# Performance work log

Hardware: AMD Instinct MI355X
Metric: run time of the kernel (lower is better)

## Reference

```python
import jax, jax.numpy as jnp
import numpy as np

N = 50000; E = 800000; G = 256; F = 34; D = 128; H = 4; C = 32; L = 4
EPS = 1e-5

def _bn(x, g, b):
    # BatchNorm1d with batch statistics (train-mode math), eval dropout (identity)
    m = jnp.mean(x, 0); v = jnp.var(x, 0)
    return g * (x - m) * jax.lax.rsqrt(v + EPS) + b

def _seg_softmax(s, seg, n):
    # numerically-stable softmax over edges grouped by destination node
    m = jax.ops.segment_max(s, seg, num_segments=n)
    m = jnp.where(jnp.isfinite(m), m, 0.0)
    e = jnp.exp(s - m[seg])
    d = jax.ops.segment_sum(e, seg, num_segments=n)
    return e / (d[seg] + 1e-16)

def setup_inputs():
    key = jax.random.key(0)
    ks = iter(jax.random.split(key, 64))
    def rn(shape, s=0.05):
        return jax.random.normal(next(ks), shape, dtype=jnp.float32) * s
    inp = {}
    inp['x'] = jax.random.normal(next(ks), (N, F), dtype=jnp.float32)
    inp['edge_index'] = jax.random.randint(next(ks), (2, E), 0, N, dtype=jnp.int32)
    inp['batch'] = jnp.sort(jax.random.randint(next(ks), (N,), 0, G, dtype=jnp.int32))
    inp['emb_W'] = rn((F, D)); inp['emb_b'] = rn((D,))
    inp['emb_g'] = jnp.ones((D,)); inp['emb_be'] = jnp.zeros((D,))
    inp['gWl'] = rn((L, D, D)); inp['gWr'] = rn((L, D, D))
    inp['gbl'] = rn((L, D)); inp['gbr'] = rn((L, D))
    inp['gatt'] = rn((L, H, C)); inp['gbias'] = rn((L, D))
    inp['gg'] = jnp.ones((L, D)); inp['gbe'] = jnp.zeros((L, D))
    inp['tWq'] = rn((D, D)); inp['tWk'] = rn((D, D)); inp['tWv'] = rn((D, D)); inp['tWs'] = rn((D, D))
    inp['tbq'] = rn((D,)); inp['tbk'] = rn((D,)); inp['tbv'] = rn((D,)); inp['tbs'] = rn((D,))
    inp['tg'] = jnp.ones((D,)); inp['tbe'] = jnp.zeros((D,))
    inp['oW1'] = rn((2 * D, D)); inp['ob1'] = rn((D,))
    inp['og'] = jnp.ones((D,)); inp['obe'] = jnp.zeros((D,))
    inp['oW2'] = rn((D, D // 2)); inp['ob2'] = rn((D // 2,))
    inp['oW3'] = rn((D // 2, 1)); inp['ob3'] = rn((1,))
    return inp

def reference(x, edge_index, batch, emb_W, emb_b, emb_g, emb_be, gWl, gWr, gbl, gbr, gatt, gbias, gg, gbe, tWq, tWk, tWv, tWs, tbq, tbk, tbv, tbs, tg, tbe, oW1, ob1, og, obe, oW2, ob2, oW3, ob3):
    x = jax.nn.relu(_bn(x @ emb_W + emb_b, emb_g, emb_be))
    sl = jnp.arange(N, dtype=edge_index.dtype)
    ei = jnp.concatenate([edge_index, jnp.stack([sl, sl])], axis=1)  # GATv2 default add_self_loops=True
    src, dst = ei[0], ei[1]
    for l in range(L):  # 4 structurally identical GATv2 layers
        xl = (x @ gWl[l] + gbl[l]).reshape(N, H, C)
        xr = (x @ gWr[l] + gbr[l]).reshape(N, H, C)
        e = jax.nn.leaky_relu(xl[src] + xr[dst], 0.2)  # [E+N, H, C]
        sc = jnp.einsum('ehc,hc->eh', e, gatt[l])
        a = _seg_softmax(sc, dst, N)
        out = jax.ops.segment_sum(xl[src] * a[..., None], dst, num_segments=N).reshape(N, D) + gbias[l]
        x = x + jax.nn.relu(_bn(out, gg[l], gbe[l]))
    # TransformerConv: no self-loops by default, dot-product attention + root skip
    s2, d2 = edge_index[0], edge_index[1]
    q = (x @ tWq + tbq).reshape(N, H, C)
    k = (x @ tWk + tbk).reshape(N, H, C)
    v = (x @ tWv + tbv).reshape(N, H, C)
    sc = jnp.einsum('ehc,ehc->eh', q[d2], k[s2]) / np.float32(np.sqrt(C))
    a = _seg_softmax(sc, d2, N)
    agg = jax.ops.segment_sum(v[s2] * a[..., None], d2, num_segments=N).reshape(N, D)
    x = x + _bn(agg + x @ tWs + tbs, tg, tbe)
    # global mean + max pooling over graphs
    cnt = jax.ops.segment_sum(jnp.ones((N,), x.dtype), batch, num_segments=G)
    xm = jax.ops.segment_sum(x, batch, num_segments=G) / jnp.maximum(cnt, 1.0)[:, None]
    xx = jax.ops.segment_max(x, batch, num_segments=G)
    xx = jnp.where(jnp.isfinite(xx), xx, 0.0)  # guard empty segments
    h = jnp.concatenate([xm, xx], axis=1)
    h = jax.nn.relu(_bn(h @ oW1 + ob1, og, obe))
    h = jax.nn.relu(h @ oW2 + ob2)
    return h @ oW3 + ob3
```

## Files before the change

### kernel.cpp

```cpp
#include <hip/hip_runtime.h>
#include <hip/hip_fp16.h>

namespace {
constexpr int NN = 50000;
constexpr int NE = 800000;
constexpr int NG = 256;
constexpr int NF = 34;
constexpr int NL = 4;
constexpr int NB = (NN + 255) / 256;
constexpr int STS = 32;
}
#define EPSB 1e-5f
#define LSLOPE 0.2f
#define INV_SQRT_C 0.17677669529663687f

typedef short bf16x8 __attribute__((ext_vector_type(8)));
typedef float f32x4 __attribute__((ext_vector_type(4)));
typedef _Float16 hv2 __attribute__((ext_vector_type(2)));

static __device__ __forceinline__ short f2bf(float f) {
    unsigned int u = __float_as_uint(f);
    u = (u + 0x7fff + ((u >> 16) & 1)) >> 16;
    return (short)u;
}
static __device__ __forceinline__ unsigned fenc(float x) {
    unsigned u = __float_as_uint(x);
    return (u & 0x80000000u) ? ~u : (u | 0x80000000u);
}
static __device__ __forceinline__ float fdec(unsigned u) {
    return __uint_as_float((u & 0x80000000u) ? (u ^ 0x80000000u) : ~u);
}
static __device__ __forceinline__ float fdot2(hv2 a, hv2 b, float c) {
    return __builtin_amdgcn_fdot2(a, b, c, false);
}

__global__ __launch_bounds__(256) void k_deg(const int* __restrict__ ei,
                                             int* __restrict__ deg,
                                             int* __restrict__ rank) {
    int tid = blockIdx.x * 256 + threadIdx.x;
    const int S = (NE + 3) / 4;
    if (tid >= S) return;
#pragma unroll
    for (int k = 0; k < 4; ++k) {
        int e = tid + k * S;
        if (e < NE) rank[e] = atomicAdd(&deg[ei[NE + e]], 1);
    }
}

__global__ __launch_bounds__(256) void k_scan1(const int* __restrict__ deg, int* __restrict__ bsum) {
    __shared__ int sm[256];
    int i = blockIdx.x * 256 + threadIdx.x;
    sm[threadIdx.x] = (i < NN) ? deg[i] : 0;
    __syncthreads();
    for (int off = 128; off > 0; off >>= 1) {
        if (threadIdx.x < off) sm[threadIdx.x] += sm[threadIdx.x + off];
        __syncthreads();
    }
    if (threadIdx.x == 0) bsum[blockIdx.x] = sm[0];
}

__global__ __launch_bounds__(256) void k_scan2(const int* __restrict__ bsum,
// ... 38 lines not shown
    int tid = blockIdx.x * 256 + threadIdx.x;
    const int S = (NE + 3) / 4;
    if (tid >= S) return;
#pragma unroll
    for (int k = 0; k < 4; ++k) {
        int e = tid + k * S;
        if (e < NE) {
            int s = ei[e];
            int d = ei[NE + e];
            int p = rp[d] + rank[e];
            esrc[p] = s;
        }
    }
}

__global__ __launch_bounds__(256) void k_prep(const float* __restrict__ gWl,
                                              const float* __restrict__ gWr,
                                              const float* __restrict__ tWq,
                                              const float* __restrict__ tWk,
                                              const float* __restrict__ tWv,
                                              const float* __restrict__ tWs,
                                              short* __restrict__ dst) {
    int m = blockIdx.x;
    const float* src;
    if (m < 4) src = gWl + m * 16384;
    else if (m < 8) src = gWr + (m - 4) * 16384;
    else if (m == 8) src = tWq;
    else if (m == 9) src = tWk;
    else if (m == 10) src = tWv;
    else src = tWs;
    short* d = dst + m * 16384;
    for (int i = threadIdx.x; i < 16384; i += 256) {
        int n = i >> 7, k = i & 127;
        d[i] = f2bf(src[k * 128 + n]);
    }
}

__global__ __launch_bounds__(256) void k_stats(const float* __restrict__ src, int nRows,
                                               float* __restrict__ st) {
    int c = threadIdx.x & 127;
    int sub = threadIdx.x >> 7;
    int r0 = blockIdx.x * 128;
    int rend = r0 + 128; if (rend > nRows) rend = nRows;
    float s = 0.f, ss = 0.f;
    for (int r = r0 + sub; r < rend; r += 2) {
        float v = src[(size_t)r * 128 + c];
        s += v; ss += v * v;
    }
    float* dst = st + (blockIdx.x & (STS - 1)) * 256;
    atomicAdd(&dst[c], s);
    atomicAdd(&dst[128 + c], ss);
}

template <int OUTH0, int OUTH1, int RES, int XOUT>
__global__ __launch_bounds__(256) void k_gemm2bn(const float* __restrict__ src,
                                                 const float* __restrict__ res,
                                                 float* __restrict__ xout,
                                                 const float* __restrict__ st,
                                                 const float* __restrict__ g,
                                                 const float* __restrict__ b,
                                                 const short* __restrict__ Wt0,
                                                 const short* __restrict__ Wt1,
                                                 const float* __restrict__ bias0,
                                                 const float* __restrict__ bias1,
                                                 void* __restrict__ out0,
                                                 void* __restrict__ out1, int nRows) {
    __shared__ short As[128 * 136];
    __shared__ short Bs[128 * 136];
    __shared__ float scsh[256];
    const float invn = 1.f / NN;
    if (threadIdx.x < 128) {
        int c = threadIdx.x;
        float s0v = 0.f, s1v = 0.f;
#pragma unroll 8
        for (int k2 = 0; k2 < STS; ++k2) {
            s0v += st[k2 * 256 + c];
            s1v += st[k2 * 256 + 128 + c];
        }
        float mean = s0v * invn;
        float var = fmaxf(s1v * invn - mean * mean, 0.f);
        float s = g[c] * rsqrtf(var + EPSB);
        scsh[c] = s;
        scsh[128 + c] = b[c] - mean * s;
    }
    {
        const int4* Wt4 = (const int4*)Wt0;
        for (int idx = threadIdx.x; idx < 2048; idx += 256) {
            int row = idx >> 4, c8 = idx & 15;
            *(int4*)&Bs[row * 136 + c8 * 8] = Wt4[idx];
        }
    }
    __syncthreads();
    int r0 = blockIdx.x * 128;
    int rows = nRows - r0; if (rows > 128) rows = 128;
    for (int idx = threadIdx.x; idx < 2048; idx += 256) {
        int r = idx >> 4, c8 = idx & 15;
        short4 sa = {0, 0, 0, 0}, sb = {0, 0, 0, 0};
        if (r < rows) {
            size_t base = (size_t)(r0 + r) * 128 + c8 * 8;
            float4 v0 = *(const float4*)&src[base];
            float4 v1 = *(const float4*)&src[base + 4];
            int c = c8 * 8;
            v0.x = fmaxf(v0.x * scsh[c + 0] + scsh[128 + c + 0], 0.f);
            v0.y = fmaxf(v0.y * scsh[c + 1] + scsh[128 + c + 1], 0.f);
            v0.z = fmaxf(v0.z * scsh[c + 2] + scsh[128 + c + 2], 0.f);
            v0.w = fmaxf(v0.w * scsh[c + 3] + scsh[128 + c + 3], 0.f);
            v1.x = fmaxf(v1.x * scsh[c + 4] + scsh[128 + c + 4], 0.f);
            v1.y = fmaxf(v1.y * scsh[c + 5] + scsh[128 + c + 5], 0.f);
            v1.z = fmaxf(v1.z * scsh[c + 6] + scsh[128 + c + 6], 0.f);
            v1.w = fmaxf(v1.w * scsh[c + 7] + scsh[128 + c + 7], 0.f);
            if (RES) {
                float4 rr0 = *(const float4*)&res[base];
                float4 rr1 = *(const float4*)&res[base + 4];
                v0.x += rr0.x; v0.y += rr0.y; v0.z += rr0.z; v0.w += rr0.w;
                v1.x += rr1.x; v1.y += rr1.y; v1.z += rr1.z; v1.w += rr1.w;
            }
            if (XOUT) {
                *(float4*)&xout[base] = v0;
                *(float4*)&xout[base + 4] = v1;
            }
            sa.x = f2bf(v0.x); sa.y = f2bf(v0.y); sa.z = f2bf(v0.z); sa.w = f2bf(v0.w);
            sb.x = f2bf(v1.x); sb.y = f2bf(v1.y); sb.z = f2bf(v1.z); sb.w = f2bf(v1.w);
        }
        *(short4*)&As[r * 136 + c8 * 8] = sa;
        *(short4*)&As[r * 136 + c8 * 8 + 4] = sb;
    }
    __syncthreads();
    int lane = threadIdx.x & 63, wave = threadIdx.x >> 6;
    int n16 = lane & 15, quad = lane >> 4;
    bf16x8 af[2][4];
#pragma unroll
    for (int rt = 0; rt < 2; ++rt)
#pragma unroll
        for (int kc = 0; kc < 4; ++kc)
            af[rt][kc] = *(const bf16x8*)&As[(wave * 32 + rt * 16 + n16) * 136 + kc * 32 + quad * 8];

    f32x4 acc[2][8];
#pragma unroll
    for (int rt = 0; rt < 2; ++rt)
#pragma unroll
        for (int ct = 0; ct < 8; ++ct) acc[rt][ct] = (f32x4){0.f, 0.f, 0.f, 0.f};
#pragma unroll
    for (int ct = 0; ct < 8; ++ct)
#pragma unroll
        for (int kc = 0; kc < 4; ++kc) {
            bf16x8 bf = *(const bf16x8*)&Bs[(ct * 16 + n16) * 136 + kc * 32 + quad * 8];
            acc[0][ct] = __builtin_amdgcn_mfma_f32_16x16x32_bf16(af[0][kc], bf, acc[0][ct], 0, 0, 0);
            acc[1][ct] = __builtin_amdgcn_mfma_f32_16x16x32_bf16(af[1][kc], bf, acc[1][ct], 0, 0, 0);
        }
#pragma unroll
    for (int ct = 0; ct < 8; ++ct) {
        int colI = ct * 16 + n16;
        float bv = bias0[colI];
#pragma unroll
        for (int rt = 0; rt < 2; ++rt)
#pragma unroll
            for (int reg = 0; reg < 4; ++reg) {
                int r = wave * 32 + rt * 16 + quad * 4 + reg;
                if (r < rows) {
                    float v = acc[rt][ct][reg] + bv;
                    if (OUTH0) ((__half*)out0)[(size_t)(r0 + r) * 128 + colI] = __float2half(v);
                    else       ((float*)out0)[(size_t)(r0 + r) * 128 + colI] = v;
                }
            }
    }
    __syncthreads();
    {
        const int4* Wt4 = (const int4*)Wt1;
        for (int idx = threadIdx.x; idx < 2048; idx += 256) {
            int row = idx >> 4, c8 = idx & 15;
            *(int4*)&Bs[row * 136 + c8 * 8] = Wt4[idx];
        }
    }
    __syncthreads();
#pragma unroll
    for (int rt = 0; rt < 2; ++rt)
#pragma unroll
        for (int ct = 0; ct < 8; ++ct) acc[rt][ct] = (f32x4){0.f, 0.f, 0.f, 0.f};
#pragma unroll
    for (int ct = 0; ct < 8; ++ct)
#pragma unroll
        for (int kc = 0; kc < 4; ++kc) {
            bf16x8 bf = *(const bf16x8*)&Bs[(ct * 16 + n16) * 136 + kc * 32 + quad * 8];
            acc[0][ct] = __builtin_amdgcn_mfma_f32_16x16x32_bf16(af[0][kc], bf, acc[0][ct], 0, 0, 0);
            acc[1][ct] = __builtin_amdgcn_mfma_f32_16x16x32_bf16(af[1][kc], bf, acc[1][ct], 0, 0, 0);
        }
#pragma unroll
    for (int ct = 0; ct < 8; ++ct) {
        int colI = ct * 16 + n16;
        float bv = bias1[colI];
#pragma unroll
        for (int rt = 0; rt < 2; ++rt)
#pragma unroll
            for (int reg = 0; reg < 4; ++reg) {
                int r = wave * 32 + rt * 16 + quad * 4 + reg;
                if (r < rows) {
                    float v = acc[rt][ct][reg] + bv;
                    if (OUTH1) ((__half*)out1)[(size_t)(r0 + r) * 128 + colI] = __float2half(v);
                    else       ((float*)out1)[(size_t)(r0 + r) * 128 + colI] = v;
                }
            }
    }
}

__global__ __launch_bounds__(256) void k_gemm4bn(const float* __restrict__ src,
                                                 const float* __restrict__ res,
                                                 float* __restrict__ xout,
                                                 const float* __restrict__ st,
                                                 const float* __restrict__ g,
                                                 const float* __restrict__ b,
                                                 const short* __restrict__ Wt,
                                                 const float* __restrict__ bq,
                                                 const float* __restrict__ bk,
                                                 const float* __restrict__ bv,
                                                 const float* __restrict__ bs,
                                                 __half* __restrict__ oq,
                                                 __half* __restrict__ ok,
                                                 __half* __restrict__ ov,
                                                 __half* __restrict__ os, int nRows) {
    __shared__ short As[128 * 136];
    __shared__ short Bs[128 * 136];
    __shared__ float scsh[256];
    const float invn = 1.f / NN;
    if (threadIdx.x < 128) {
        int c = threadIdx.x;
        float s0v = 0.f, s1v = 0.f;
#pragma unroll 8
        for (int k2 = 0; k2 < STS; ++k2) {
            s0v += st[k2 * 256 + c];
            s1v += st[k2 * 256 + 128 + c];
        }
        float mean = s0v * invn;
        float var = fmaxf(s1v * invn - mean * mean, 0.f);
        float s = g[c] * rsqrtf(var + EPSB);
        scsh[c] = s;
        scsh[128 + c] = b[c] - mean * s;
    }
    __syncthreads();
    int r0 = blockIdx.x * 128;
    int rows = nRows - r0; if (rows > 128) rows = 128;
    for (int idx = threadIdx.x; idx < 2048; idx += 256) {
        int r = idx >> 4, c8 = idx & 15;
        short4 sa = {0, 0, 0, 0}, sb = {0, 0, 0, 0};
        if (r < rows) {
            size_t base = (size_t)(r0 + r) * 128 + c8 * 8;
            float4 v0 = *(const float4*)&src[base];
            float4 v1 = *(const float4*)&src[base + 4];
            int c = c8 * 8;
            v0.x = fmaxf(v0.x * scsh[c + 0] + scsh[128 + c + 0], 0.f);
            v0.y = fmaxf(v0.y * scsh[c + 1] + scsh[128 + c + 1], 0.f);
            v0.z = fmaxf(v0.z * scsh[c + 2] + scsh[128 + c + 2], 0.f);
            v0.w = fmaxf(v0.w * scsh[c + 3] + scsh[128 + c + 3], 0.f);
            v1.x = fmaxf(v1.x * scsh[c + 4] + scsh[128 + c + 4], 0.f);
            v1.y = fmaxf(v1.y * scsh[c + 5] + scsh[128 + c + 5], 0.f);
            v1.z = fmaxf(v1.z * scsh[c + 6] + scsh[128 + c + 6], 0.f);
            v1.w = fmaxf(v1.w * scsh[c + 7] + scsh[128 + c + 7], 0.f);
            float4 rr0 = *(const float4*)&res[base];
            float4 rr1 = *(const float4*)&res[base + 4];
            v0.x += rr0.x; v0.y += rr0.y; v0.z += rr0.z; v0.w += rr0.w;
            v1.x += rr1.x; v1.y += rr1.y; v1.z += rr1.z; v1.w += rr1.w;
            *(float4*)&xout[base] = v0;
            *(float4*)&xout[base + 4] = v1;
            sa.x = f2bf(v0.x); sa.y = f2bf(v0.y); sa.z = f2bf(v0.z); sa.w = f2bf(v0.w);
            sb.x = f2bf(v1.x); sb.y = f2bf(v1.y); sb.z = f2bf(v1.z); sb.w = f2bf(v1.w);
        }
        *(short4*)&As[r * 136 + c8 * 8] = sa;
        *(short4*)&As[r * 136 + c8 * 8 + 4] = sb;
    }
    int lane = threadIdx.x & 63, wave = threadIdx.x >> 6;
    int n16 = lane & 15, quad = lane >> 4;
    __half* outs[4] = {oq, ok, ov, os};
    const float* biases[4] = {bq, bk, bv, bs};
    bf16x8 af[2][4];
    bool afLoaded = false;
    for (int m = 0; m < 4; ++m) {
        {
            const int4* Wt4 = (const int4*)(Wt + (size_t)m * 16384);
            for (int idx = threadIdx.x; idx < 2048; idx += 256) {
                int row = idx >> 4, c8 = idx & 15;
                *(int4*)&Bs[row * 136 + c8 * 8] = Wt4[idx];
            }
        }
        __syncthreads();
        if (!afLoaded) {
            afLoaded = true;
#pragma unroll
            for (int rt = 0; rt < 2; ++rt)
#pragma unroll
                for (int kc = 0; kc < 4; ++kc)
                    af[rt][kc] = *(const bf16x8*)&As[(wave * 32 + rt * 16 + n16) * 136 + kc * 32 + quad * 8];
        }
        f32x4 acc[2][8];
#pragma unroll
        for (int rt = 0; rt < 2; ++rt)
#pragma unroll
            for (int ct = 0; ct < 8; ++ct) acc[rt][ct] = (f32x4){0.f, 0.f, 0.f, 0.f};
#pragma unroll
        for (int ct = 0; ct < 8; ++ct)
#pragma unroll
            for (int kc = 0; kc < 4; ++kc) {
                bf16x8 bf = *(const bf16x8*)&Bs[(ct * 16 + n16) * 136 + kc * 32 + quad * 8];
                acc[0][ct] = __builtin_amdgcn_mfma_f32_16x16x32_bf16(af[0][kc], bf, acc[0][ct], 0, 0, 0);
                acc[1][ct] = __builtin_amdgcn_mfma_f32_16x16x32_bf16(af[1][kc], bf, acc[1][ct], 0, 0, 0);
            }
        __half* om = outs[m];
        const float* bm = biases[m];
#pragma unroll
        for (int ct = 0; ct < 8; ++ct) {
            int colI = ct * 16 + n16;
            float bv2 = bm[colI];
#pragma unroll
            for (int rt = 0; rt < 2; ++rt)
#pragma unroll
                for (int reg = 0; reg < 4; ++reg) {
                    int r = wave * 32 + rt * 16 + quad * 4 + reg;
                    if (r < rows)
                        om[(size_t)(r0 + r) * 128 + colI] = __float2half(acc[rt][ct][reg] + bv2);
                }
        }
        if (m < 3) __syncthreads();
    }
}

__global__ __launch_bounds__(256) void k_gemm_emb(const float* __restrict__ A,
                                                  const float* __restrict__ W,
                                                  const float* __restrict__ bias,
                                                  float* __restrict__ out, int nRows,
                                                  float* __restrict__ stms) {
    __shared__ float As[64 * NF];
    __shared__ float sred[256];
    int r0 = blockIdx.x * 64;
    int rows = nRows - r0; if (rows > 64) rows = 64;
    int total = rows * NF;
    for (int idx = threadIdx.x; idx < 64 * NF; idx += 256)
        As[idx] = (idx < total) ? A[(size_t)r0 * NF + idx] : 0.f;
    sred[threadIdx.x] = 0.f;
    __syncthreads();
    int tx = threadIdx.x & 31, ty = threadIdx.x >> 5;
    const float4* W4 = (const float4*)W;
    float acc[8][4];
#pragma unroll
    for (int j = 0; j < 8; ++j)
#pragma unroll
        for (int i = 0; i < 4; ++i) acc[j][i] = 0.f;
#pragma unroll 2
    for (int k = 0; k < NF; ++k) {
        float4 w = W4[k * 32 + tx];
#pragma unroll
        for (int j = 0; j < 8; ++j) {
            float a = As[(ty * 8 + j) * NF + k];
            acc[j][0] += a * w.x; acc[j][1] += a * w.y;
            acc[j][2] += a * w.z; acc[j][3] += a * w.w;
        }
    }
    float4 b = ((const float4*)bias)[tx];
    float s[4] = {0.f, 0.f, 0.f, 0.f}, ss[4] = {0.f, 0.f, 0.f, 0.f};
#pragma unroll
    for (int j = 0; j < 8; ++j) {
        int r = ty * 8 + j;
        if (r < rows) {
            float4 o = make_float4(acc[j][0] + b.x, acc[j][1] + b.y,
                                   acc[j][2] + b.z, acc[j][3] + b.w);
            ((float4*)out)[(size_t)(r0 + r) * 32 + tx] = o;
            s[0] += o.x; ss[0] += o.x * o.x;
            s[1] += o.y; ss[1] += o.y * o.y;
            s[2] += o.z; ss[2] += o.z * o.z;
            s[3] += o.w; ss[3] += o.w * o.w;
        }
    }
#pragma unroll
    for (int i = 0; i < 4; ++i) {
        atomicAdd(&sred[tx * 4 + i], s[i]);
        atomicAdd(&sred[128 + tx * 4 + i], ss[i]);
    }
    __syncthreads();
    atomicAdd(&stms[(blockIdx.x & (STS - 1)) * 256 + threadIdx.x], sred[threadIdx.x]);
}

__global__ __launch_bounds__(256) void k_gat_aggr(const __half* __restrict__ xl,
                                                  const __half* __restrict__ xr,
                                                  const float* __restrict__ att,
                                                  const float* __restrict__ gbias_l,
                                                  const int* __restrict__ rp,
                                                  const int* __restrict__ esrc,
                                                  float* __restrict__ out) {
    int lane = threadIdx.x & 63;
    int node = blockIdx.x * 4 + (threadIdx.x >> 6);
    if (node >= NN) return;
    int q = lane >> 4;
    int l16 = lane & 15;
    int c8 = l16 * 8;
    float4 xrr = *(const float4*)&xr[(unsigned)node * 128u + c8];
    hv2 xrh[4] = {*(hv2*)&xrr.x, *(hv2*)&xrr.y, *(hv2*)&xrr.z, *(hv2*)&xrr.w};
    float4 atA = *(const float4*)&att[c8];
    float4 atB = *(const float4*)&att[c8 + 4];
    hv2 ath[4] = {{(_Float16)atA.x, (_Float16)atA.y}, {(_Float16)atA.z, (_Float16)atA.w},
                  {(_Float16)atB.x, (_Float16)atB.y}, {(_Float16)atB.z, (_Float16)atB.w}};
    const hv2 hz = {(_Float16)0.f, (_Float16)0.f};
    const hv2 hs = {(_Float16)LSLOPE, (_Float16)LSLOPE};
    int s0 = rp[node];
// ... 20 lines not shown
            a[2 * k + 1] += w * (float)f[k].y;
        }
        l += w;
    };
    int j = q;
    for (; j + 12 < T; j += 16) { body(j); body(j + 4); body(j + 8); body(j + 12); }
    for (; j + 4 < T; j += 8) { body(j); body(j + 4); }
    for (; j < T; j += 4) body(j);
#pragma unroll
    for (int k = 0; k < 8; ++k) { a[k] += __shfl_xor(a[k], 16); a[k] += __shfl_xor(a[k], 32); }
    l += __shfl_xor(l, 16); l += __shfl_xor(l, 32);
    if (q == 0) {
        float inv = 1.f / (l + 1e-16f);
        float4 gb0 = *(const float4*)&gbias_l[c8];
        float4 gb1 = *(const float4*)&gbias_l[c8 + 4];
        float4 o0 = make_float4(a[0] * inv + gb0.x, a[1] * inv + gb0.y,
                                a[2] * inv + gb0.z, a[3] * inv + gb0.w);
        float4 o1 = make_float4(a[4] * inv + gb1.x, a[5] * inv + gb1.y,
                                a[6] * inv + gb1.z, a[7] * inv + gb1.w);
        *(float4*)&out[(unsigned)node * 128u + c8] = o0;
        *(float4*)&out[(unsigned)node * 128u + c8 + 4] = o1;
    }
}

__global__ __launch_bounds__(256) void k_trans_aggr(const __half* __restrict__ qh,
                                                    const __half* __restrict__ kh,
                                                    const __half* __restrict__ vv,
                                                    const __half* __restrict__ sT,
                                                    const int* __restrict__ rp,
                                                    const int* __restrict__ esrc,
                                                    float* __restrict__ out) {
    int lane = threadIdx.x & 63;
    int node = blockIdx.x * 4 + (threadIdx.x >> 6);
    if (node >= NN) return;
    int q = lane >> 4;
    int l16 = lane & 15;
    int c8 = l16 * 8;
    float4 qr = *(const float4*)&qh[(unsigned)node * 128u + c8];
    const hv2 hinv = {(_Float16)INV_SQRT_C, (_Float16)INV_SQRT_C};
    hv2 qv[4] = {(*(hv2*)&qr.x) * hinv, (*(hv2*)&qr.y) * hinv,
                 (*(hv2*)&qr.z) * hinv, (*(hv2*)&qr.w) * hinv};
    int s0 = rp[node];
    int T = rp[node + 1] - s0;
    float a[8] = {0.f, 0.f, 0.f, 0.f, 0.f, 0.f, 0.f, 0.f};
    float l = 0.f;
    auto body = [&](int j) {
// ... 13 lines not shown
            a[2 * k + 1] += w * (float)vvv[k].y;
        }
        l += w;
    };
    int j = q;
    for (; j + 12 < T; j += 16) { body(j); body(j + 4); body(j + 8); body(j + 12); }
    for (; j + 4 < T; j += 8) { body(j); body(j + 4); }
    for (; j < T; j += 4) body(j);
#pragma unroll
    for (int k = 0; k < 8; ++k) { a[k] += __shfl_xor(a[k], 16); a[k] += __shfl_xor(a[k], 32); }
    l += __shfl_xor(l, 16); l += __shfl_xor(l, 32);
    if (q == 0) {
        float inv = 1.f / (l + 1e-16f);
        float4 straw = *(const float4*)&sT[(unsigned)node * 128u + c8];
        hv2 st[4] = {*(hv2*)&straw.x, *(hv2*)&straw.y, *(hv2*)&straw.z, *(hv2*)&straw.w};
        float4 o0 = make_float4(a[0] * inv + (float)st[0].x, a[1] * inv + (float)st[0].y,
                                a[2] * inv + (float)st[1].x, a[3] * inv + (float)st[1].y);
        float4 o1 = make_float4(a[4] * inv + (float)st[2].x, a[5] * inv + (float)st[2].y,
                                a[6] * inv + (float)st[3].x, a[7] * inv + (float)st[3].y);
        *(float4*)&out[(unsigned)node * 128u + c8] = o0;
        *(float4*)&out[(unsigned)node * 128u + c8 + 4] = o1;
    }
}

__global__ __launch_bounds__(256) void k_pool_part(const float* __restrict__ src,
                                                   const float* __restrict__ res,
                                                   const float* __restrict__ st,
                                                   const float* __restrict__ g,
                                                   const float* __restrict__ b,
                                                   const int* __restrict__ batch,
                                                   float* __restrict__ psum,
                                                   unsigned* __restrict__ pmax) {
    __shared__ int bs[64];
    __shared__ float sc_sh[128], sh_sh[128];
    int r0 = blockIdx.x * 64;
    if (threadIdx.x < 64) {
        int r = r0 + threadIdx.x;
        bs[threadIdx.x] = (r < NN) ? batch[r] : -1;
    }
    const float invn = 1.f / NN;
// ... 17 lines not shown
    float scv = sc_sh[c];
    float shv = sh_sh[c];
    int curg = -1;
    float s = 0.f, fmx = -INFINITY;
    for (int i = sub; i < 64; i += 2) {
        int r = r0 + i;
        if (r >= NN) break;
        int gr = bs[i];
        if (gr != curg) {
            if (curg >= 0) {
                atomicAdd(&psum[curg * 128 + c], s);
                atomicMax(&pmax[curg * 128 + c], fenc(fmx));
            }
            curg = gr; s = 0.f; fmx = -INFINITY;
        }
        float v = src[(size_t)r * 128 + c] * scv + shv + res[(size_t)r * 128 + c];
        s += v; fmx = fmaxf(fmx, v);
    }
    if (curg >= 0) {
        atomicAdd(&psum[curg * 128 + c], s);
        atomicMax(&pmax[curg * 128 + c], fenc(fmx));
    }
}

__global__ __launch_bounds__(128) void k_pool_head1(const float* __restrict__ psum,
                                                    const unsigned* __restrict__ pmax,
                                                    const int* __restrict__ batch,
                                                    const float* __restrict__ W,
                                                    const float* __restrict__ b,
                                                    float* __restrict__ t1,
                                                    float* __restrict__ st6) {
// ... 106 lines not shown
    __half* xrh  = xlh + NDsz;
    __half* vh   = xrh + NDsz;
    __half* sh   = vh + NDsz;
    short* Wt    = (short*)(sh + NDsz);
    int* deg     = (int*)(Wt + 12 * 16384);
    int* rp      = deg + NN;
    int* cursor  = rp + NN + 1;
    int2* edg    = (int2*)(cursor + NN);
    int* bsum    = (int*)(edg + NE + 64);
    int* boff    = bsum + 256;
    float* psum  = (float*)(boff + 256);
    unsigned* pmax = (unsigned*)(psum + NG * 128);
    int* rank    = (int*)scb;
    int* esrc    = (int*)edg;
    float* stms  = scb + NE;

    hipMemsetAsync(deg, 0, NN * sizeof(int), stream);
    hipMemsetAsync(stats + 6 * 256, 0, 256 * sizeof(float), stream);
    hipMemsetAsync(stms, 0, 6 * STS * 256 * sizeof(float), stream);
    hipMemsetAsync(psum, 0, NG * 128 * 2 * sizeof(float), stream);

    k_prep<<<12, 256, 0, stream>>>(gWl, gWr, tWq, tWk, tWv, tWs, Wt);

    const int S4 = (NE + 3) / 4;
    const int gQuarter = (S4 + 255) / 256;
    k_deg<<<gQuarter, 256, 0, stream>>>(ei, deg, rank);
    k_scan1<<<NB, 256, 0, stream>>>(deg, bsum);
    k_scan2<<<1, 256, 0, stream>>>(bsum, boff, rp);
    k_scan3<<<NB, 256, 0, stream>>>(deg, boff, rp);
    k_fill<<<gQuarter, 256, 0, stream>>>(ei, rp, rank, esrc);

    const int gEmb  = (NN + 63) / 64;
    const int gGemm = (NN + 127) / 128;
    const int gStat = (NN + 127) / 128;
    const int gNode = (NN + 3) / 4;
    const int gPool = (NN + 63) / 64;
    const int REG = STS * 256;

    k_gemm_emb<<<gEmb, 256, 0, stream>>>(x_in, emb_W, emb_b, bA, NN, stms + 0 * REG);

    k_gemm2bn<1, 1, 0, 1><<<gGemm, 256, 0, stream>>>(bA, nullptr, x, stms + 0 * REG, emb_g, emb_be,
                                                     Wt + (size_t)0 * 16384, Wt + (size_t)4 * 16384,
                                                     gbl + 0 * 128, gbr + 0 * 128, xlh, xrh, NN);
    k_gat_aggr<<<gNode, 256, 0, stream>>>(xlh, xrh, gatt + 0 * 128, gbias + 0 * 128, rp, esrc, bC);
    k_stats<<<gStat, 256, 0, stream>>>(bC, NN, stms + 1 * REG);
    k_gemm2bn<1, 1, 1, 1><<<gGemm, 256, 0, stream>>>(bC, x, bA, stms + 1 * REG, gg + 0 * 128, gbe + 0 * 128,
                                                     Wt + (size_t)1 * 16384, Wt + (size_t)5 * 16384,
                                                     gbl + 1 * 128, gbr + 1 * 128, xlh, xrh, NN);
    k_gat_aggr<<<gNode, 256, 0, stream>>>(xlh, xrh, gatt + 1 * 128, gbias + 1 * 128, rp, esrc, bC);
    k_stats<<<gStat, 256, 0, stream>>>(bC, NN, stms + 2 * REG);
    k_gemm2bn<1, 1, 1, 1><<<gGemm, 256, 0, stream>>>(bC, bA, x, stms + 2 * REG, gg + 1 * 128, gbe + 1 * 128,
                                                     Wt + (size_t)2 * 16384, Wt + (size_t)6 * 16384,
                                                     gbl + 2 * 128, gbr + 2 * 128, xlh, xrh, NN);
    k_gat_aggr<<<gNode, 256, 0, stream>>>(xlh, xrh, gatt + 2 * 128, gbias + 2 * 128, rp, esrc, bC);
    k_stats<<<gStat, 256, 0, stream>>>(bC, NN, stms + 3 * REG);
    k_gemm2bn<1, 1, 1, 1><<<gGemm, 256, 0, stream>>>(bC, x, bA, stms + 3 * REG, gg + 2 * 128, gbe + 2 * 128,
                                                     Wt + (size_t)3 * 16384, Wt + (size_t)7 * 16384,
                                                     gbl + 3 * 128, gbr + 3 * 128, xlh, xrh, NN);
    k_gat_aggr<<<gNode, 256, 0, stream>>>(xlh, xrh, gatt + 3 * 128, gbias + 3 * 128, rp, esrc, bC);
    k_stats<<<gStat, 256, 0, stream>>>(bC, NN, stms + 4 * REG);

    k_gemm4bn<<<gGemm, 256, 0, stream>>>(bC, bA, x, stms + 4 * REG, gg + 3 * 128, gbe + 3 * 128,
                                         Wt + (size_t)8 * 16384, tbq, tbk, tbv, tbs,
                                         xrh, xlh, vh, sh, NN);
    k_trans_aggr<<<gNode, 256, 0, stream>>>(xrh, xlh, vh, sh, rp, esrc, bC);
    k_stats<<<gStat, 256, 0, stream>>>(bC, NN, stms + 5 * REG);

    k_pool_part<<<gPool, 256, 0, stream>>>(bC, x, stms + 5 * REG, tg, tbe, batch, psum, pmax);
    k_pool_head1<<<NG, 128, 0, stream>>>(psum, pmax, batch, oW1, ob1, t1, stats + 6 * 256);
    k_head2<<<NG, 64, 0, stream>>>(t1, stats + 6 * 256, og, obe, oW2, ob2, oW3, ob3, out);
}
```

Measured before the change: 821.8 us.

## Store aggregation outputs in fp16, halve GEMM row tiles, merge init kernels

```diff
diff --git a/kernel.cpp b/kernel.cpp
--- a/kernel.cpp
+++ b/kernel.cpp
@@ -9,6 +9,8 @@
 constexpr int NL = 4;
 constexpr int NB = (NN + 255) / 256;
 constexpr int STS = 32;
+constexpr int GQ = ((NE + 3) / 4 + 255) / 256;
+constexpr int GE = (NN + 63) / 64;
 }
 #define EPSB 1e-5f
 #define LSLOPE 0.2f
@@ -34,17 +36,98 @@
     return __builtin_amdgcn_fdot2(a, b, c, false);
 }
 
-__global__ __launch_bounds__(256) void k_deg(const int* __restrict__ ei,
-                                             int* __restrict__ deg,
-                                             int* __restrict__ rank) {
-    int tid = blockIdx.x * 256 + threadIdx.x;
-    const int S = (NE + 3) / 4;
-    if (tid >= S) return;
-#pragma unroll
-    for (int k = 0; k < 4; ++k) {
-        int e = tid + k * S;
-        if (e < NE) rank[e] = atomicAdd(&deg[ei[NE + e]], 1);
-    }
+__global__ __launch_bounds__(256) void k_init(const int* __restrict__ ei,
+                                              int* __restrict__ deg,
+                                              int* __restrict__ rank,
+                                              const float* __restrict__ gWl,
+                                              const float* __restrict__ gWr,
+                                              const float* __restrict__ tWq,
+                                              const float* __restrict__ tWk,
+                                              const float* __restrict__ tWv,
+                                              const float* __restrict__ tWs,
+                                              short* __restrict__ Wt,
+                                              const float* __restrict__ A,
+                                              const float* __restrict__ W,
+                                              const float* __restrict__ bias,
+                                              float* __restrict__ outEmb,
+                                              float* __restrict__ stms) {
+    __shared__ float As[64 * NF];
+    __shared__ float sred[256];
+    int blk = blockIdx.x;
+    if (blk < GQ) {
+        int tid = blk * 256 + threadIdx.x;
+        const int S = (NE + 3) / 4;
+        if (tid >= S) return;
+#pragma unroll
+        for (int k = 0; k < 4; ++k) {
+            int e = tid + k * S;
+            if (e < NE) rank[e] = atomicAdd(&deg[ei[NE + e]], 1);
+        }
+        return;
+    }
+    blk -= GQ;
+    if (blk < 12) {
+        const float* src;
+        if (blk < 4) src = gWl + blk * 16384;
+        else if (blk < 8) src = gWr + (blk - 4) * 16384;
+        else if (blk == 8) src = tWq;
+        else if (blk == 9) src = tWk;
+        else if (blk == 10) src = tWv;
+        else src = tWs;
+        short* d = Wt + blk * 16384;
+        for (int i = threadIdx.x; i < 16384; i += 256) {
+            int n = i >> 7, k = i & 127;
+            d[i] = f2bf(src[k * 128 + n]);
+        }
+        return;
+    }
+    blk -= 12;
+    int r0 = blk * 64;
+    int rows = NN - r0; if (rows > 64) rows = 64;
+    int total = rows * NF;
+    for (int idx = threadIdx.x; idx < 64 * NF; idx += 256)
+        As[idx] = (idx < total) ? A[(size_t)r0 * NF + idx] : 0.f;
+    sred[threadIdx.x] = 0.f;
+    __syncthreads();
+    int tx = threadIdx.x & 31, ty = threadIdx.x >> 5;
+    const float4* W4 = (const float4*)W;
+    float acc[8][4];
+#pragma unroll
+    for (int j = 0; j < 8; ++j)
+#pragma unroll
+        for (int i = 0; i < 4; ++i) acc[j][i] = 0.f;
+#pragma unroll 2
+    for (int k = 0; k < NF; ++k) {
+        float4 w = W4[k * 32 + tx];
+#pragma unroll
+        for (int j = 0; j < 8; ++j) {
+            float a = As[(ty * 8 + j) * NF + k];
+            acc[j][0] += a * w.x; acc[j][1] += a * w.y;
+            acc[j][2] += a * w.z; acc[j][3] += a * w.w;
+        }
+    }
+    float4 b = ((const float4*)bias)[tx];
+    float s[4] = {0.f, 0.f, 0.f, 0.f}, ss[4] = {0.f, 0.f, 0.f, 0.f};
+#pragma unroll
+    for (int j = 0; j < 8; ++j) {
+        int r = ty * 8 + j;
+        if (r < rows) {
+            float4 o = make_float4(acc[j][0] + b.x, acc[j][1] + b.y,
+                                   acc[j][2] + b.z, acc[j][3] + b.w);
+            ((float4*)outEmb)[(size_t)(r0 + r) * 32 + tx] = o;
+            s[0] += o.x; ss[0] += o.x * o.x;
+            s[1] += o.y; ss[1] += o.y * o.y;
+            s[2] += o.z; ss[2] += o.z * o.z;
+            s[3] += o.w; ss[3] += o.w * o.w;
+        }
+    }
+#pragma unroll
+    for (int i = 0; i < 4; ++i) {
+        atomicAdd(&sred[tx * 4 + i], s[i]);
+        atomicAdd(&sred[128 + tx * 4 + i], ss[i]);
+    }
+    __syncthreads();
+    atomicAdd(&stms[(blk & (STS - 1)) * 256 + threadIdx.x], sred[threadIdx.x]);
 }
 
 __global__ __launch_bounds__(256) void k_scan1(const int* __restrict__ deg, int* __restrict__ bsum) {
@@ -113,29 +196,7 @@
     }
 }
 
-__global__ __launch_bounds__(256) void k_prep(const float* __restrict__ gWl,
-                                              const float* __restrict__ gWr,
-                                              const float* __restrict__ tWq,
-                                              const float* __restrict__ tWk,
-                                              const float* __restrict__ tWv,
-                                              const float* __restrict__ tWs,
-                                              short* __restrict__ dst) {
-    int m = blockIdx.x;
-    const float* src;
-    if (m < 4) src = gWl + m * 16384;
-    else if (m < 8) src = gWr + (m - 4) * 16384;
-    else if (m == 8) src = tWq;
-    else if (m == 9) src = tWk;
-    else if (m == 10) src = tWv;
-    else src = tWs;
-    short* d = dst + m * 16384;
-    for (int i = threadIdx.x; i < 16384; i += 256) {
-        int n = i >> 7, k = i & 127;
-        d[i] = f2bf(src[k * 128 + n]);
-    }
-}
-
-__global__ __launch_bounds__(256) void k_stats(const float* __restrict__ src, int nRows,
+__global__ __launch_bounds__(256) void k_stats(const __half* __restrict__ src, int nRows,
                                                float* __restrict__ st) {
     int c = threadIdx.x & 127;
     int sub = threadIdx.x >> 7;
@@ -143,7 +204,7 @@
     int rend = r0 + 128; if (rend > nRows) rend = nRows;
     float s = 0.f, ss = 0.f;
     for (int r = r0 + sub; r < rend; r += 2) {
-        float v = src[(size_t)r * 128 + c];
+        float v = __half2float(src[(size_t)r * 128 + c]);
         s += v; ss += v * v;
     }
     float* dst = st + (blockIdx.x & (STS - 1)) * 256;
@@ -151,7 +212,7 @@
     atomicAdd(&dst[128 + c], ss);
 }
 
-template <int OUTH0, int OUTH1, int RES, int XOUT>
+template <int SRC16, int OUTH0, int OUTH1, int RES, int XOUT>
 __global__ __launch_bounds__(256) void k_gemm2bn(const float* __restrict__ src,
                                                  const float* __restrict__ res,
                                                  float* __restrict__ xout,
@@ -164,7 +225,7 @@
                                                  const float* __restrict__ bias1,
                                                  void* __restrict__ out0,
                                                  void* __restrict__ out1, int nRows) {
-    __shared__ short As[128 * 136];
+    __shared__ short As[64 * 136];
     __shared__ short Bs[128 * 136];
     __shared__ float scsh[256];
     const float invn = 1.f / NN;
@@ -190,15 +251,25 @@
         }
     }
     __syncthreads();
-    int r0 = blockIdx.x * 128;
-    int rows = nRows - r0; if (rows > 128) rows = 128;
-    for (int idx = threadIdx.x; idx < 2048; idx += 256) {
+    int r0 = blockIdx.x * 64;
+    int rows = nRows - r0; if (rows > 64) rows = 64;
+    for (int idx = threadIdx.x; idx < 1024; idx += 256) {
         int r = idx >> 4, c8 = idx & 15;
         short4 sa = {0, 0, 0, 0}, sb = {0, 0, 0, 0};
         if (r < rows) {
             size_t base = (size_t)(r0 + r) * 128 + c8 * 8;
-            float4 v0 = *(const float4*)&src[base];
-            float4 v1 = *(const float4*)&src[base + 4];
+            float4 v0, v1;
+            if (SRC16) {
+                union { float4 f4; __half h[8]; } u;
+                u.f4 = *(const float4*)&((const __half*)src)[base];
+                v0 = make_float4(__half2float(u.h[0]), __half2float(u.h[1]),
+                                 __half2float(u.h[2]), __half2float(u.h[3]));
+                v1 = make_float4(__half2float(u.h[4]), __half2float(u.h[5]),
+                                 __half2float(u.h[6]), __half2float(u.h[7]));
+            } else {
+                v0 = *(const float4*)&src[base];
+                v1 = *(const float4*)&src[base + 4];
+            }
             int c = c8 * 8;
             v0.x = fmaxf(v0.x * scsh[c + 0] + scsh[128 + c + 0], 0.f);
             v0.y = fmaxf(v0.y * scsh[c + 1] + scsh[128 + c + 1], 0.f);
@@ -227,41 +298,34 @@
     __syncthreads();
     int lane = threadIdx.x & 63, wave = threadIdx.x >> 6;
     int n16 = lane & 15, quad = lane >> 4;
-    bf16x8 af[2][4];
-#pragma unroll
-    for (int rt = 0; rt < 2; ++rt)
-#pragma unroll
-        for (int kc = 0; kc < 4; ++kc)
-            af[rt][kc] = *(const bf16x8*)&As[(wave * 32 + rt * 16 + n16) * 136 + kc * 32 + quad * 8];
-
-    f32x4 acc[2][8];
-#pragma unroll
-    for (int rt = 0; rt < 2; ++rt)
-#pragma unroll
-        for (int ct = 0; ct < 8; ++ct) acc[rt][ct] = (f32x4){0.f, 0.f, 0.f, 0.f};
+    bf16x8 af[4];
+#pragma unroll
+    for (int kc = 0; kc < 4; ++kc)
+        af[kc] = *(const bf16x8*)&As[(wave * 16 + n16) * 136 + kc * 32 + quad * 8];
+
+    f32x4 acc[8];
+#pragma unroll
+    for (int ct = 0; ct < 8; ++ct) acc[ct] = (f32x4){0.f, 0.f, 0.f, 0.f};
 #pragma unroll
     for (int ct = 0; ct < 8; ++ct)
 #pragma unroll
         for (int kc = 0; kc < 4; ++kc) {
             bf16x8 bf = *(const bf16x8*)&Bs[(ct * 16 + n16) * 136 + kc * 32 + quad * 8];
-            acc[0][ct] = __builtin_amdgcn_mfma_f32_16x16x32_bf16(af[0][kc], bf, acc[0][ct], 0, 0, 0);
-            acc[1][ct] = __builtin_amdgcn_mfma_f32_16x16x32_bf16(af[1][kc], bf, acc[1][ct], 0, 0, 0);
+            acc[ct] = __builtin_amdgcn_mfma_f32_16x16x32_bf16(af[kc], bf, acc[ct], 0, 0, 0);
         }
 #pragma unroll
     for (int ct = 0; ct < 8; ++ct) {
         int colI = ct * 16 + n16;
         float bv = bias0[colI];
 #pragma unroll
-        for (int rt = 0; rt < 2; ++rt)
-#pragma unroll
-            for (int reg = 0; reg < 4; ++reg) {
-                int r = wave * 32 + rt * 16 + quad * 4 + reg;
-                if (r < rows) {
-                    float v = acc[rt][ct][reg] + bv;
-                    if (OUTH0) ((__half*)out0)[(size_t)(r0 + r) * 128 + colI] = __float2half(v);
-                    else       ((float*)out0)[(size_t)(r0 + r) * 128 + colI] = v;
-                }
+        for (int reg = 0; reg < 4; ++reg) {
+            int r = wave * 16 + quad * 4 + reg;
+            if (r < rows) {
+                float v = acc[ct][reg] + bv;
+                if (OUTH0) ((__half*)out0)[(size_t)(r0 + r) * 128 + colI] = __float2half(v);
+                else       ((float*)out0)[(size_t)(r0 + r) * 128 + colI] = v;
             }
+        }
     }
     __syncthreads();
     {
@@ -273,36 +337,31 @@
     }
     __syncthreads();
 #pragma unroll
-    for (int rt = 0; rt < 2; ++rt)
-#pragma unroll
-        for (int ct = 0; ct < 8; ++ct) acc[rt][ct] = (f32x4){0.f, 0.f, 0.f, 0.f};
+    for (int ct = 0; ct < 8; ++ct) acc[ct] = (f32x4){0.f, 0.f, 0.f, 0.f};
 #pragma unroll
     for (int ct = 0; ct < 8; ++ct)
 #pragma unroll
         for (int kc = 0; kc < 4; ++kc) {
             bf16x8 bf = *(const bf16x8*)&Bs[(ct * 16 + n16) * 136 + kc * 32 + quad * 8];
-            acc[0][ct] = __builtin_amdgcn_mfma_f32_16x16x32_bf16(af[0][kc], bf, acc[0][ct], 0, 0, 0);
-            acc[1][ct] = __builtin_amdgcn_mfma_f32_16x16x32_bf16(af[1][kc], bf, acc[1][ct], 0, 0, 0);
+            acc[ct] = __builtin_amdgcn_mfma_f32_16x16x32_bf16(af[kc], bf, acc[ct], 0, 0, 0);
         }
 #pragma unroll
     for (int ct = 0; ct < 8; ++ct) {
         int colI = ct * 16 + n16;
         float bv = bias1[colI];
 #pragma unroll
-        for (int rt = 0; rt < 2; ++rt)
-#pragma unroll
-            for (int reg = 0; reg < 4; ++reg) {
-                int r = wave * 32 + rt * 16 + quad * 4 + reg;
-                if (r < rows) {
-                    float v = acc[rt][ct][reg] + bv;
-                    if (OUTH1) ((__half*)out1)[(size_t)(r0 + r) * 128 + colI] = __float2half(v);
-                    else       ((float*)out1)[(size_t)(r0 + r) * 128 + colI] = v;
-                }
+        for (int reg = 0; reg < 4; ++reg) {
+            int r = wave * 16 + quad * 4 + reg;
+            if (r < rows) {
+                float v = acc[ct][reg] + bv;
+                if (OUTH1) ((__half*)out1)[(size_t)(r0 + r) * 128 + colI] = __float2half(v);
+                else       ((float*)out1)[(size_t)(r0 + r) * 128 + colI] = v;
             }
-    }
-}
-
-__global__ __launch_bounds__(256) void k_gemm4bn(const float* __restrict__ src,
+        }
+    }
+}
+
+__global__ __launch_bounds__(256) void k_gemm4bn(const __half* __restrict__ src,
                                                  const float* __restrict__ res,
                                                  float* __restrict__ xout,
                                                  const float* __restrict__ st,
@@ -317,7 +376,7 @@
                                                  __half* __restrict__ ok,
                                                  __half* __restrict__ ov,
                                                  __half* __restrict__ os, int nRows) {
-    __shared__ short As[128 * 136];
+    __shared__ short As[64 * 136];
     __shared__ short Bs[128 * 136];
     __shared__ float scsh[256];
     const float invn = 1.f / NN;
@@ -336,15 +395,19 @@
         scsh[128 + c] = b[c] - mean * s;
     }
     __syncthreads();
-    int r0 = blockIdx.x * 128;
-    int rows = nRows - r0; if (rows > 128) rows = 128;
-    for (int idx = threadIdx.x; idx < 2048; idx += 256) {
+    int r0 = blockIdx.x * 64;
+    int rows = nRows - r0; if (rows > 64) rows = 64;
+    for (int idx = threadIdx.x; idx < 1024; idx += 256) {
         int r = idx >> 4, c8 = idx & 15;
         short4 sa = {0, 0, 0, 0}, sb = {0, 0, 0, 0};
         if (r < rows) {
             size_t base = (size_t)(r0 + r) * 128 + c8 * 8;
-            float4 v0 = *(const float4*)&src[base];
-            float4 v1 = *(const float4*)&src[base + 4];
+            union { float4 f4; __half h[8]; } u;
+            u.f4 = *(const float4*)&src[base];
+            float4 v0 = make_float4(__half2float(u.h[0]), __half2float(u.h[1]),
+                                    __half2float(u.h[2]), __half2float(u.h[3]));
+            float4 v1 = make_float4(__half2float(u.h[4]), __half2float(u.h[5]),
+                                    __half2float(u.h[6]), __half2float(u.h[7]));
             int c = c8 * 8;
             v0.x = fmaxf(v0.x * scsh[c + 0] + scsh[128 + c + 0], 0.f);
             v0.y = fmaxf(v0.y * scsh[c + 1] + scsh[128 + c + 1], 0.f);
@@ -370,7 +433,7 @@
     int n16 = lane & 15, quad = lane >> 4;
     __half* outs[4] = {oq, ok, ov, os};
     const float* biases[4] = {bq, bk, bv, bs};
-    bf16x8 af[2][4];
+    bf16x8 af[4];
     bool afLoaded = false;
     for (int m = 0; m < 4; ++m) {
         {
@@ -384,23 +447,18 @@
         if (!afLoaded) {
             afLoaded = true;
 #pragma unroll
-            for (int rt = 0; rt < 2; ++rt)
-#pragma unroll
-                for (int kc = 0; kc < 4; ++kc)
-                    af[rt][kc] = *(const bf16x8*)&As[(wave * 32 + rt * 16 + n16) * 136 + kc * 32 + quad * 8];
-        }
-        f32x4 acc[2][8];
-#pragma unroll
-        for (int rt = 0; rt < 2; ++rt)
-#pragma unroll
-            for (int ct = 0; ct < 8; ++ct) acc[rt][ct] = (f32x4){0.f, 0.f, 0.f, 0.f};
+            for (int kc = 0; kc < 4; ++kc)
+                af[kc] = *(const bf16x8*)&As[(wave * 16 + n16) * 136 + kc * 32 + quad * 8];
+        }
+        f32x4 acc[8];
+#pragma unroll
+        for (int ct = 0; ct < 8; ++ct) acc[ct] = (f32x4){0.f, 0.f, 0.f, 0.f};
 #pragma unroll
         for (int ct = 0; ct < 8; ++ct)
 #pragma unroll
             for (int kc = 0; kc < 4; ++kc) {
                 bf16x8 bf = *(const bf16x8*)&Bs[(ct * 16 + n16) * 136 + kc * 32 + quad * 8];
-                acc[0][ct] = __builtin_amdgcn_mfma_f32_16x16x32_bf16(af[0][kc], bf, acc[0][ct], 0, 0, 0);
-                acc[1][ct] = __builtin_amdgcn_mfma_f32_16x16x32_bf16(af[1][kc], bf, acc[1][ct], 0, 0, 0);
+                acc[ct] = __builtin_amdgcn_mfma_f32_16x16x32_bf16(af[kc], bf, acc[ct], 0, 0, 0);
             }
         __half* om = outs[m];
         const float* bm = biases[m];
@@ -409,71 +467,14 @@
             int colI = ct * 16 + n16;
             float bv2 = bm[colI];
 #pragma unroll
-            for (int rt = 0; rt < 2; ++rt)
-#pragma unroll
-                for (int reg = 0; reg < 4; ++reg) {
-                    int r = wave * 32 + rt * 16 + quad * 4 + reg;
-                    if (r < rows)
-                        om[(size_t)(r0 + r) * 128 + colI] = __float2half(acc[rt][ct][reg] + bv2);
-                }
+            for (int reg = 0; reg < 4; ++reg) {
+                int r = wave * 16 + quad * 4 + reg;
+                if (r < rows)
+                    om[(size_t)(r0 + r) * 128 + colI] = __float2half(acc[ct][reg] + bv2);
+            }
         }
         if (m < 3) __syncthreads();
     }
-}
-
-__global__ __launch_bounds__(256) void k_gemm_emb(const float* __restrict__ A,
-                                                  const float* __restrict__ W,
-                                                  const float* __restrict__ bias,
-                                                  float* __restrict__ out, int nRows,
-                                                  float* __restrict__ stms) {
-    __shared__ float As[64 * NF];
-    __shared__ float sred[256];
-    int r0 = blockIdx.x * 64;
-    int rows = nRows - r0; if (rows > 64) rows = 64;
-    int total = rows * NF;
-    for (int idx = threadIdx.x; idx < 64 * NF; idx += 256)
-        As[idx] = (idx < total) ? A[(size_t)r0 * NF + idx] : 0.f;
-    sred[threadIdx.x] = 0.f;
-    __syncthreads();
-    int tx = threadIdx.x & 31, ty = threadIdx.x >> 5;
-    const float4* W4 = (const float4*)W;
-    float acc[8][4];
-#pragma unroll
-    for (int j = 0; j < 8; ++j)
-#pragma unroll
-        for (int i = 0; i < 4; ++i) acc[j][i] = 0.f;
-#pragma unroll 2
-    for (int k = 0; k < NF; ++k) {
-        float4 w = W4[k * 32 + tx];
-#pragma unroll
-        for (int j = 0; j < 8; ++j) {
-            float a = As[(ty * 8 + j) * NF + k];
-            acc[j][0] += a * w.x; acc[j][1] += a * w.y;
-            acc[j][2] += a * w.z; acc[j][3] += a * w.w;
-        }
-    }
-    float4 b = ((const float4*)bias)[tx];
-    float s[4] = {0.f, 0.f, 0.f, 0.f}, ss[4] = {0.f, 0.f, 0.f, 0.f};
-#pragma unroll
-    for (int j = 0; j < 8; ++j) {
-        int r = ty * 8 + j;
-        if (r < rows) {
-            float4 o = make_float4(acc[j][0] + b.x, acc[j][1] + b.y,
-                                   acc[j][2] + b.z, acc[j][3] + b.w);
-            ((float4*)out)[(size_t)(r0 + r) * 32 + tx] = o;
-            s[0] += o.x; ss[0] += o.x * o.x;
-            s[1] += o.y; ss[1] += o.y * o.y;
-            s[2] += o.z; ss[2] += o.z * o.z;
-            s[3] += o.w; ss[3] += o.w * o.w;
-        }
-    }
-#pragma unroll
-    for (int i = 0; i < 4; ++i) {
-        atomicAdd(&sred[tx * 4 + i], s[i]);
-        atomicAdd(&sred[128 + tx * 4 + i], ss[i]);
-    }
-    __syncthreads();
-    atomicAdd(&stms[(blockIdx.x & (STS - 1)) * 256 + threadIdx.x], sred[threadIdx.x]);
 }
 
 __global__ __launch_bounds__(256) void k_gat_aggr(const __half* __restrict__ xl,
@@ -482,7 +483,7 @@
                                                   const float* __restrict__ gbias_l,
                                                   const int* __restrict__ rp,
                                                   const int* __restrict__ esrc,
-                                                  float* __restrict__ out) {
+                                                  __half* __restrict__ out) {
     int lane = threadIdx.x & 63;
     int node = blockIdx.x * 4 + (threadIdx.x >> 6);
     if (node >= NN) return;
@@ -533,12 +534,12 @@
         float inv = 1.f / (l + 1e-16f);
         float4 gb0 = *(const float4*)&gbias_l[c8];
         float4 gb1 = *(const float4*)&gbias_l[c8 + 4];
-        float4 o0 = make_float4(a[0] * inv + gb0.x, a[1] * inv + gb0.y,
-                                a[2] * inv + gb0.z, a[3] * inv + gb0.w);
-        float4 o1 = make_float4(a[4] * inv + gb1.x, a[5] * inv + gb1.y,
-                                a[6] * inv + gb1.z, a[7] * inv + gb1.w);
-        *(float4*)&out[(unsigned)node * 128u + c8] = o0;
-        *(float4*)&out[(unsigned)node * 128u + c8 + 4] = o1;
+        union { float4 f4; __half h[8]; } u;
+        u.h[0] = __float2half(a[0] * inv + gb0.x); u.h[1] = __float2half(a[1] * inv + gb0.y);
+        u.h[2] = __float2half(a[2] * inv + gb0.z); u.h[3] = __float2half(a[3] * inv + gb0.w);
+        u.h[4] = __float2half(a[4] * inv + gb1.x); u.h[5] = __float2half(a[5] * inv + gb1.y);
+        u.h[6] = __float2half(a[6] * inv + gb1.z); u.h[7] = __float2half(a[7] * inv + gb1.w);
+        *(float4*)&out[(unsigned)node * 128u + c8] = u.f4;
     }
 }
 
@@ -548,7 +549,7 @@
                                                     const __half* __restrict__ sT,
                                                     const int* __restrict__ rp,
                                                     const int* __restrict__ esrc,
-                                                    float* __restrict__ out) {
+                                                    __half* __restrict__ out) {
     int lane = threadIdx.x & 63;
     int node = blockIdx.x * 4 + (threadIdx.x >> 6);
     if (node >= NN) return;
@@ -592,16 +593,20 @@
         float inv = 1.f / (l + 1e-16f);
         float4 straw = *(const float4*)&sT[(unsigned)node * 128u + c8];
         hv2 st[4] = {*(hv2*)&straw.x, *(hv2*)&straw.y, *(hv2*)&straw.z, *(hv2*)&straw.w};
-        float4 o0 = make_float4(a[0] * inv + (float)st[0].x, a[1] * inv + (float)st[0].y,
-                                a[2] * inv + (float)st[1].x, a[3] * inv + (float)st[1].y);
-        float4 o1 = make_float4(a[4] * inv + (float)st[2].x, a[5] * inv + (float)st[2].y,
-                                a[6] * inv + (float)st[3].x, a[7] * inv + (float)st[3].y);
-        *(float4*)&out[(unsigned)node * 128u + c8] = o0;
-        *(float4*)&out[(unsigned)node * 128u + c8 + 4] = o1;
-    }
-}
-
-__global__ __launch_bounds__(256) void k_pool_part(const float* __restrict__ src,
+        union { float4 f4; __half h[8]; } u;
+        u.h[0] = __float2half(a[0] * inv + (float)st[0].x);
+        u.h[1] = __float2half(a[1] * inv + (float)st[0].y);
+        u.h[2] = __float2half(a[2] * inv + (float)st[1].x);
+        u.h[3] = __float2half(a[3] * inv + (float)st[1].y);
+        u.h[4] = __float2half(a[4] * inv + (float)st[2].x);
+        u.h[5] = __float2half(a[5] * inv + (float)st[2].y);
+        u.h[6] = __float2half(a[6] * inv + (float)st[3].x);
+        u.h[7] = __float2half(a[7] * inv + (float)st[3].y);
+        *(float4*)&out[(unsigned)node * 128u + c8] = u.f4;
+    }
+}
+
+__global__ __launch_bounds__(256) void k_pool_part(const __half* __restrict__ src,
                                                    const float* __restrict__ res,
                                                    const float* __restrict__ st,
                                                    const float* __restrict__ g,
@@ -649,7 +654,7 @@
             }
             curg = gr; s = 0.f; fmx = -INFINITY;
         }
-        float v = src[(size_t)r * 128 + c] * scv + shv + res[(size_t)r * 128 + c];
+        float v = __half2float(src[(size_t)r * 128 + c]) * scv + shv + res[(size_t)r * 128 + c];
         s += v; fmx = fmaxf(fmx, v);
     }
     if (curg >= 0) {
@@ -786,59 +791,55 @@
     int* rank    = (int*)scb;
     int* esrc    = (int*)edg;
     float* stms  = scb + NE;
+    __half* bCh  = (__half*)bC;
 
     hipMemsetAsync(deg, 0, NN * sizeof(int), stream);
     hipMemsetAsync(stats + 6 * 256, 0, 256 * sizeof(float), stream);
     hipMemsetAsync(stms, 0, 6 * STS * 256 * sizeof(float), stream);
     hipMemsetAsync(psum, 0, NG * 128 * 2 * sizeof(float), stream);
 
-    k_prep<<<12, 256, 0, stream>>>(gWl, gWr, tWq, tWk, tWv, tWs, Wt);
-
-    const int S4 = (NE + 3) / 4;
-    const int gQuarter = (S4 + 255) / 256;
-    k_deg<<<gQuarter, 256, 0, stream>>>(ei, deg, rank);
-    k_scan1<<<NB, 256, 0, stream>>>(deg, bsum);
-    k_scan2<<<1, 256, 0, stream>>>(bsum, boff, rp);
-    k_scan3<<<NB, 256, 0, stream>>>(deg, boff, rp);
-    k_fill<<<gQuarter, 256, 0, stream>>>(ei, rp, rank, esrc);
-
-    const int gEmb  = (NN + 63) / 64;
-    const int gGemm = (NN + 127) / 128;
+    const int gGemm = (NN + 63) / 64;
     const int gStat = (NN + 127) / 128;
     const int gNode = (NN + 3) / 4;
     const int gPool = (NN + 63) / 64;
     const int REG = STS * 256;
 
-    k_gemm_emb<<<gEmb, 256, 0, stream>>>(x_in, emb_W, emb_b, bA, NN, stms + 0 * REG);
-
-    k_gemm2bn<1, 1, 0, 1><<<gGemm, 256, 0, stream>>>(bA, nullptr, x, stms + 0 * REG, emb_g, emb_be,
-                                                     Wt + (size_t)0 * 16384, Wt + (size_t)4 * 16384,
-                                                     gbl + 0 * 128, gbr + 0 * 128, xlh, xrh, NN);
-    k_gat_aggr<<<gNode, 256, 0, stream>>>(xlh, xrh, gatt + 0 * 128, gbias + 0 * 128, rp, esrc, bC);
-    k_stats<<<gStat, 256, 0, stream>>>(bC, NN, stms + 1 * REG);
-    k_gemm2bn<1, 1, 1, 1><<<gGemm, 256, 0, stream>>>(bC, x, bA, stms + 1 * REG, gg + 0 * 128, gbe + 0 * 128,
-                                                     Wt + (size_t)1 * 16384, Wt + (size_t)5 * 16384,
-                                                     gbl + 1 * 128, gbr + 1 * 128, xlh, xrh, NN);
-    k_gat_aggr<<<gNode, 256, 0, stream>>>(xlh, xrh, gatt + 1 * 128, gbias + 1 * 128, rp, esrc, bC);
-    k_stats<<<gStat, 256, 0, stream>>>(bC, NN, stms + 2 * REG);
-    k_gemm2bn<1, 1, 1, 1><<<gGemm, 256, 0, stream>>>(bC, bA, x, stms + 2 * REG, gg + 1 * 128, gbe + 1 * 128,
-                                                     Wt + (size_t)2 * 16384, Wt + (size_t)6 * 16384,
-                                                     gbl + 2 * 128, gbr + 2 * 128, xlh, xrh, NN);
-    k_gat_aggr<<<gNode, 256, 0, stream>>>(xlh, xrh, gatt + 2 * 128, gbias + 2 * 128, rp, esrc, bC);
-    k_stats<<<gStat, 256, 0, stream>>>(bC, NN, stms + 3 * REG);
-    k_gemm2bn<1, 1, 1, 1><<<gGemm, 256, 0, stream>>>(bC, x, bA, stms + 3 * REG, gg + 2 * 128, gbe + 2 * 128,
-                                                     Wt + (size_t)3 * 16384, Wt + (size_t)7 * 16384,
-                                                     gbl + 3 * 128, gbr + 3 * 128, xlh, xrh, NN);
-    k_gat_aggr<<<gNode, 256, 0, stream>>>(xlh, xrh, gatt + 3 * 128, gbias + 3 * 128, rp, esrc, bC);
-    k_stats<<<gStat, 256, 0, stream>>>(bC, NN, stms + 4 * REG);
-
-    k_gemm4bn<<<gGemm, 256, 0, stream>>>(bC, bA, x, stms + 4 * REG, gg + 3 * 128, gbe + 3 * 128,
+    k_init<<<GQ + 12 + GE, 256, 0, stream>>>(ei, deg, rank, gWl, gWr, tWq, tWk, tWv, tWs,
+                                             Wt, x_in, emb_W, emb_b, bA, stms + 0 * REG);
+
+    k_scan1<<<NB, 256, 0, stream>>>(deg, bsum);
+    k_scan2<<<1, 256, 0, stream>>>(bsum, boff, rp);
+    k_scan3<<<NB, 256, 0, stream>>>(deg, boff, rp);
+    k_fill<<<GQ, 256, 0, stream>>>(ei, rp, rank, esrc);
+
+    k_gemm2bn<0, 1, 1, 0, 1><<<gGemm, 256, 0, stream>>>(bA, nullptr, x, stms + 0 * REG, emb_g, emb_be,
+                                                        Wt + (size_t)0 * 16384, Wt + (size_t)4 * 16384,
+                                                        gbl + 0 * 128, gbr + 0 * 128, xlh, xrh, NN);
+    k_gat_aggr<<<gNode, 256, 0, stream>>>(xlh, xrh, gatt + 0 * 128, gbias + 0 * 128, rp, esrc, bCh);
+    k_stats<<<gStat, 256, 0, stream>>>(bCh, NN, stms + 1 * REG);
+    k_gemm2bn<1, 1, 1, 1, 1><<<gGemm, 256, 0, stream>>>((const float*)bCh, x, bA, stms + 1 * REG, gg + 0 * 128, gbe + 0 * 128,
+                                                        Wt + (size_t)1 * 16384, Wt + (size_t)5 * 16384,
+                                                        gbl + 1 * 128, gbr + 1 * 128, xlh, xrh, NN);
+    k_gat_aggr<<<gNode, 256, 0, stream>>>(xlh, xrh, gatt + 1 * 128, gbias + 1 * 128, rp, esrc, bCh);
+    k_stats<<<gStat, 256, 0, stream>>>(bCh, NN, stms + 2 * REG);
+    k_gemm2bn<1, 1, 1, 1, 1><<<gGemm, 256, 0, stream>>>((const float*)bCh, bA, x, stms + 2 * REG, gg + 1 * 128, gbe + 1 * 128,
+                                                        Wt + (size_t)2 * 16384, Wt + (size_t)6 * 16384,
+                                                        gbl + 2 * 128, gbr + 2 * 128, xlh, xrh, NN);
+    k_gat_aggr<<<gNode, 256, 0, stream>>>(xlh, xrh, gatt + 2 * 128, gbias + 2 * 128, rp, esrc, bCh);
+    k_stats<<<gStat, 256, 0, stream>>>(bCh, NN, stms + 3 * REG);
+    k_gemm2bn<1, 1, 1, 1, 1><<<gGemm, 256, 0, stream>>>((const float*)bCh, x, bA, stms + 3 * REG, gg + 2 * 128, gbe + 2 * 128,
+                                                        Wt + (size_t)3 * 16384, Wt + (size_t)7 * 16384,
+                                                        gbl + 3 * 128, gbr + 3 * 128, xlh, xrh, NN);
+    k_gat_aggr<<<gNode, 256, 0, stream>>>(xlh, xrh, gatt + 3 * 128, gbias + 3 * 128, rp, esrc, bCh);
+    k_stats<<<gStat, 256, 0, stream>>>(bCh, NN, stms + 4 * REG);
+
+    k_gemm4bn<<<gGemm, 256, 0, stream>>>(bCh, bA, x, stms + 4 * REG, gg + 3 * 128, gbe + 3 * 128,
                                          Wt + (size_t)8 * 16384, tbq, tbk, tbv, tbs,
                                          xrh, xlh, vh, sh, NN);
-    k_trans_aggr<<<gNode, 256, 0, stream>>>(xrh, xlh, vh, sh, rp, esrc, bC);
-    k_stats<<<gStat, 256, 0, stream>>>(bC, NN, stms + 5 * REG);
-
-    k_pool_part<<<gPool, 256, 0, stream>>>(bC, x, stms + 5 * REG, tg, tbe, batch, psum, pmax);
+    k_trans_aggr<<<gNode, 256, 0, stream>>>(xrh, xlh, vh, sh, rp, esrc, bCh);
+    k_stats<<<gStat, 256, 0, stream>>>(bCh, NN, stms + 5 * REG);
+
+    k_pool_part<<<gPool, 256, 0, stream>>>(bCh, x, stms + 5 * REG, tg, tbe, batch, psum, pmax);
     k_pool_head1<<<NG, 128, 0, stream>>>(psum, pmax, batch, oW1, ob1, t1, stats + 6 * 256);
     k_head2<<<NG, 64, 0, stream>>>(t1, stats + 6 * 256, og, obe, oW2, ob2, oW3, ob3, out);
 }
```

After: 822.8 us. About the same (+0.1%).
